# Performance work log

Measured on AMD Instinct MI355X. Metric: run time of the kernel, lower is better.

Reference implementation:

```python
import jax, jax.numpy as jnp
import numpy as np

N_JOINTS = 21
EDGES = np.array([[0,13],[0,1],[0,4],[0,10],[0,7],[13,14],[14,15],[15,16],[1,2],[2,3],[3,17],[4,5],[5,6],[6,18],[10,11],[11,12],[12,19],[7,8],[8,9],[9,20]], dtype=np.int32)


def _build_adj():
    # SemGCN-style adj_mx_from_edges: symmetric adjacency + self loops, row-normalized
    A = np.zeros((N_JOINTS, N_JOINTS), np.float32)
    A[EDGES[:, 0], EDGES[:, 1]] = 1.0
    A = np.maximum(A, A.T)
    A = A + np.eye(N_JOINTS, dtype=np.float32)
    A = A / A.sum(axis=1, keepdims=True)
    return A


def setup_inputs() -> dict:
    key = jax.random.key(0)
    ks = jax.random.split(key, 8)
    B, C, Hm, Wm = 128, 235, 64, 64
    heads, fo = 4, 32
    feature_s = jax.random.normal(ks[0], (B, C, Hm, Wm), jnp.float32)
    target_s = jax.random.uniform(ks[1], (B, N_JOINTS, Hm, Wm), jnp.float32)
    bn_gamma = jnp.ones((N_JOINTS,), jnp.float32)
    bn_beta = jnp.zeros((N_JOINTS,), jnp.float32)
    gat_w = jax.random.normal(ks[2], (C, heads * fo), jnp.float32) * 0.05
    gat_att_src = jax.random.normal(ks[3], (heads, fo), jnp.float32) * 0.1
    gat_att_dst = jax.random.normal(ks[4], (heads, fo), jnp.float32) * 0.1
    gat_bias = jnp.zeros((heads * fo,), jnp.float32)
    cheb_w = jax.random.normal(ks[5], (2, heads * fo, 3), jnp.float32) * 0.05
    cheb_bias = jnp.zeros((3,), jnp.float32)
    # PyG GATConv adds self loops: 20 skeleton edges + 21 self edges = 41
    src = np.concatenate([EDGES[:, 0], np.arange(N_JOINTS, dtype=np.int32)])
    dst = np.concatenate([EDGES[:, 1], np.arange(N_JOINTS, dtype=np.int32)])
    return {
        'feature_s': feature_s, 'target_s': target_s,
        'bn_gamma': bn_gamma, 'bn_beta': bn_beta,
        'gat_w': gat_w, 'gat_att_src': gat_att_src, 'gat_att_dst': gat_att_dst,
        'gat_bias': gat_bias, 'cheb_w': cheb_w, 'cheb_bias': cheb_bias,
        'adj': jnp.asarray(_build_adj()),
        'edge_src': jnp.asarray(src), 'edge_dst': jnp.asarray(dst),
    }


def reference(feature_s, target_s, bn_gamma, bn_beta, gat_w, gat_att_src, gat_att_dst, gat_bias, cheb_w, cheb_bias, adj, edge_src, edge_dst):
    B, C = feature_s.shape[0], feature_s.shape[1]
    N = target_s.shape[1]
    # per-sample query embedding: [B, 21, HW] @ [B, HW, C] -> [B, 21, C]
    f = feature_s.reshape(B, C, -1)
    t = target_s.reshape(B, N, -1)
    q = jnp.einsum('bnp,bcp->bnc', t, f)
    # BatchNorm1d(21), training mode: normalize per joint-channel over (B, C)
    mean = q.mean(axis=(0, 2), keepdims=True)
    var = q.var(axis=(0, 2), keepdims=True)
    q = (q - mean) * jax.lax.rsqrt(var + 1e-5) * bn_gamma[None, :, None] + bn_beta[None, :, None]
    q = jnp.where(q >= 0, q, 0.1 * q)  # LeakyReLU(0.1)
    # GATConv (4 heads, 32 dims, concat) vmapped over batch of identical graphs
    heads, fo = gat_att_src.shape
    h = (q @ gat_w).reshape(B, N, heads, fo)
    a_src = jnp.einsum('bnhf,hf->bnh', h, gat_att_src)
    a_dst = jnp.einsum('bnhf,hf->bnh', h, gat_att_dst)
    e = a_src[:, edge_src] + a_dst[:, edge_dst]           # [B, E, H]
    e = jnp.where(e >= 0, e, 0.2 * e)                     # GAT default negative_slope=0.2
    seg_max = jax.vmap(lambda v: jax.ops.segment_max(v, edge_dst, num_segments=N))
    seg_sum = jax.vmap(lambda v: jax.ops.segment_sum(v, edge_dst, num_segments=N))
    m = seg_max(e)                                        # [B, N, H]
    ex = jnp.exp(e - m[:, edge_dst])
    den = seg_sum(ex)
    alpha = ex / den[:, edge_dst]                         # per-dst softmax
    msg = alpha[..., None] * h[:, edge_src]               # [B, E, H, Fo]
    out = seg_sum(msg.reshape(B, -1, heads * fo))         # [B, N, H*Fo]
    x = out + gat_bias
    # ChebConv K=2 (GraFormer-style): T0 = I, T1 = L = I - D^{-1/2} A D^{-1/2}
    d = jnp.sum(adj, axis=-1) ** -0.5
    L = jnp.eye(N, dtype=adj.dtype) - d[:, None] * adj * d[None, :]
    y = jnp.einsum('bnc,co->bno', x, cheb_w[0]) + jnp.einsum('mn,bnc,co->bmo', L, x, cheb_w[1])
    return y + cheb_bias
```

## Files before the change

kernel.cpp:

```cpp
#include <hip/hip_runtime.h>
#include <hip/hip_bf16.h>

constexpr int B  = 128;
constexpr int C  = 235;
constexpr int N  = 21;
constexpr int HW = 4096;
constexpr int HO = 128;
constexpr int E  = 41;

typedef __attribute__((ext_vector_type(8)))  short  short8;
typedef __attribute__((ext_vector_type(16))) float  f32x16;

__device__ inline unsigned short bf16r(float x) {
    return __bfloat16_as_ushort(__float2bfloat16(x));
}

constexpr int KSPLIT = 8;
constexpr int KRANGE = HW / KSPLIT;

__global__ __launch_bounds__(256) void k1_qgemm(
    const float* __restrict__ f,
    const float* __restrict__ t,
    float* __restrict__ qp)
{
    const int b    = blockIdx.y;
    const int ks   = blockIdx.x;
    const int tid  = threadIdx.x;
    const int wave = tid >> 6;
    const int lane = tid & 63;
    const int l31  = lane & 31;
    const int kh   = lane >> 5;

    const float* fb = f + (size_t)b * C * HW;
    const float* tb = t + (size_t)b * N * HW;

    const int arow = (l31 < N) ? l31 : (N - 1);
    const int c1   = wave * 64 + l31;
    const int c2   = wave * 64 + 32 + l31;
    const int c1c  = (c1 < C) ? c1 : (C - 1);
    const int c2c  = (c2 < C) ? c2 : (C - 1);

    const float* pa = tb + (size_t)arow * HW + kh * 8;
    const float* p1 = fb + (size_t)c1c  * HW + kh * 8;
    const float* p2 = fb + (size_t)c2c  * HW + kh * 8;

    f32x16 acc0 = {};
    f32x16 acc1 = {};

    const int kend = ks * KRANGE + KRANGE;
    #pragma unroll 2
    for (int k = ks * KRANGE; k < kend; k += 16) {
        const float4 alo = *reinterpret_cast<const float4*>(pa + k);
        const float4 ahi = *reinterpret_cast<const float4*>(pa + k + 4);
        const float4 b1l = *reinterpret_cast<const float4*>(p1 + k);
        const float4 b1h = *reinterpret_cast<const float4*>(p1 + k + 4);
        const float4 b2l = *reinterpret_cast<const float4*>(p2 + k);
        const float4 b2h = *reinterpret_cast<const float4*>(p2 + k + 4);

        union { short8 v; unsigned short u[8]; } av, bv1, bv2;
        av.u[0]  = bf16r(alo.x); av.u[1]  = bf16r(alo.y);
        av.u[2]  = bf16r(alo.z); av.u[3]  = bf16r(alo.w);
        av.u[4]  = bf16r(ahi.x); av.u[5]  = bf16r(ahi.y);
        av.u[6]  = bf16r(ahi.z); av.u[7]  = bf16r(ahi.w);
        bv1.u[0] = bf16r(b1l.x); bv1.u[1] = bf16r(b1l.y);
        bv1.u[2] = bf16r(b1l.z); bv1.u[3] = bf16r(b1l.w);
        bv1.u[4] = bf16r(b1h.x); bv1.u[5] = bf16r(b1h.y);
        bv1.u[6] = bf16r(b1h.z); bv1.u[7] = bf16r(b1h.w);
        bv2.u[0] = bf16r(b2l.x); bv2.u[1] = bf16r(b2l.y);
        bv2.u[2] = bf16r(b2l.z); bv2.u[3] = bf16r(b2l.w);
        bv2.u[4] = bf16r(b2h.x); bv2.u[5] = bf16r(b2h.y);
        bv2.u[6] = bf16r(b2h.z); bv2.u[7] = bf16r(b2h.w);

        acc0 = __builtin_amdgcn_mfma_f32_32x32x16_bf16(av.v, bv1.v, acc0, 0, 0, 0);
        acc1 = __builtin_amdgcn_mfma_f32_32x32x16_bf16(av.v, bv2.v, acc1, 0, 0, 0);
    }

    float* qpk = qp + ((size_t)ks * B + b) * N * C;
    #pragma unroll
    for (int reg = 0; reg < 16; reg++) {
        const int row = (reg & 3) + 8 * (reg >> 2) + 4 * kh;
        if (row < N) {
            if (c1 < C) qpk[row * C + c1] = acc0[reg];
            if (c2 < C) qpk[row * C + c2] = acc1[reg];
        }
    }
}

__global__ __launch_bounds__(256) void k1b_reduce(
    const float* __restrict__ qp, float* __restrict__ q)
{
    const int i = blockIdx.x * 256 + threadIdx.x;
    constexpr int S = B * N * C;
    if (i < S) {
        float s = 0.f;
        #pragma unroll
        for (int p = 0; p < KSPLIT; p++) s += qp[(size_t)p * S + i];
        q[i] = s;
    }
}

__global__ __launch_bounds__(256) void k2_bnstats(
    const float* __restrict__ q,
    const float* __restrict__ gamma,
    const float* __restrict__ beta,
    float* __restrict__ stats)
{
    const int n = blockIdx.x;
    const int tid = threadIdx.x;
    float s = 0.f, s2 = 0.f;
    if (tid < C) {
        for (int b = 0; b < B; b++) {
            const float v = q[((size_t)b * N + n) * C + tid];
            s += v; s2 += v * v;
        }
    }
    for (int off = 32; off; off >>= 1) {
        s  += __shfl_down(s,  off);
        s2 += __shfl_down(s2, off);
    }
    __shared__ float rs[4], rs2[4];
    const int wave = tid >> 6, lane = tid & 63;
    if (lane == 0) { rs[wave] = s; rs2[wave] = s2; }
    __syncthreads();
    if (tid == 0) {
        const float S  = rs[0] + rs[1] + rs[2] + rs[3];
        const float S2 = rs2[0] + rs2[1] + rs2[2] + rs2[3];
        const float cnt = (float)(B * C);
        const float mean = S / cnt;
        const float var  = S2 / cnt - mean * mean;
        const float scale = gamma[n] * rsqrtf(var + 1e-5f);
        stats[2 * n]     = scale;
        stats[2 * n + 1] = beta[n] - mean * scale;
    }
}

__global__ __launch_bounds__(256) void k3_tail(
    const float* __restrict__ q,
    const float* __restrict__ stats,
    const float* __restrict__ gatw,
    const float* __restrict__ attsrc,
    const float* __restrict__ attdst,
    const float* __restrict__ gatbias,
    const float* __restrict__ chebw,
    const float* __restrict__ chebbias,
    const float* __restrict__ adj,
    const int* __restrict__ esrc,
    const int* __restrict__ edst,
    float* __restrict__ out)
{
    __shared__ float ql[N][C + 1];
    __shared__ float Wl[48][HO];
    __shared__ float hl[N][HO];
    __shared__ float xl[N][HO];
    __shared__ float asrcl[N][4], adstl[N][4];
    __shared__ float el[E][4], alphal[E][4];
    __shared__ float mx[N][4], den[N][4];
    __shared__ float zl[N][3], t0l[N][3], dsl[N];
    __shared__ int esl[E], edl[E];

    const int b = blockIdx.x;
    const int tid = threadIdx.x;

    for (int v = tid; v < N * C; v += 256) {
        const int n = v / C, c = v % C;
        float x = q[((size_t)b * N + n) * C + c];
        x = x * stats[2 * n] + stats[2 * n + 1];
        ql[n][c] = (x >= 0.f) ? x : 0.1f * x;
    }
    if (tid < E) { esl[tid] = esrc[tid]; edl[tid] = edst[tid]; }
    for (int v = tid; v < N * HO; v += 256) hl[v >> 7][v & 127] = 0.f;
    __syncthreads();

    for (int k0 = 0; k0 < C; k0 += 48) {
        const int kc = (C - k0) < 48 ? (C - k0) : 48;
        for (int v = tid; v < kc * HO; v += 256) {
            const int kk = v >> 7, o = v & 127;
            Wl[kk][o] = gatw[(size_t)(k0 + kk) * HO + o];
        }
        __syncthreads();
        for (int idx = tid; idx < N * HO; idx += 256) {
            const int n = idx >> 7, o = idx & 127;
            float s = hl[n][o];
            for (int kk = 0; kk < kc; kk++)
                s += ql[n][k0 + kk] * Wl[kk][o];
            hl[n][o] = s;
        }
        __syncthreads();
    }

    if (tid < N * 4) {
        const int n = tid >> 2, h = tid & 3;
        float ss = 0.f, sd = 0.f;
        for (int fo = 0; fo < 32; fo++) {
            const float hv = hl[n][h * 32 + fo];
            ss += hv * attsrc[h * 32 + fo];
            sd += hv * attdst[h * 32 + fo];
        }
        asrcl[n][h] = ss; adstl[n][h] = sd;
    }
    __syncthreads();
    if (tid < E * 4) {
        const int e = tid >> 2, h = tid & 3;
        const float v = asrcl[esl[e]][h] + adstl[edl[e]][h];
        el[e][h] = (v >= 0.f) ? v : 0.2f * v;
    }
    __syncthreads();
    if (tid < N * 4) {
        const int n = tid >> 2, h = tid & 3;
        float m = -1e30f;
        for (int e = 0; e < E; e++)
            if (edl[e] == n) m = fmaxf(m, el[e][h]);
        mx[n][h] = m;
    }
    __syncthreads();
    if (tid < E * 4) {
        const int e = tid >> 2, h = tid & 3;
        el[e][h] = __expf(el[e][h] - mx[edl[e]][h]);
    }
    __syncthreads();
    if (tid < N * 4) {
        const int n = tid >> 2, h = tid & 3;
        float s = 0.f;
        for (int e = 0; e < E; e++)
            if (edl[e] == n) s += el[e][h];
        den[n][h] = s;
    }
    __syncthreads();
    if (tid < E * 4) {
        const int e = tid >> 2, h = tid & 3;
        alphal[e][h] = el[e][h] / den[edl[e]][h];
    }
    __syncthreads();

    for (int idx = tid; idx < N * HO; idx += 256) {
        const int n = idx >> 7, o = idx & 127, h = o >> 5;
        float s = 0.f;
        for (int e = 0; e < E; e++)
            if (edl[e] == n) s += alphal[e][h] * hl[esl[e]][o];
        xl[n][o] = s + gatbias[o];
    }
    if (tid < N) {
        float s = 0.f;
        for (int j = 0; j < N; j++) s += adj[tid * N + j];
        dsl[tid] = rsqrtf(s);
    }
    __syncthreads();

    if (tid < N * 3) {
        const int n = tid / 3, o = tid % 3;
        float s0 = 0.f, sz = 0.f;
        for (int c2 = 0; c2 < HO; c2++) {
            const float xv = xl[n][c2];
            s0 += xv * chebw[(size_t)c2 * 3 + o];
            sz += xv * chebw[(size_t)(HO + c2) * 3 + o];
        }
        t0l[n][o] = s0; zl[n][o] = sz;
    }
    __syncthreads();
    if (tid < N * 3) {
        const int m = tid / 3, o = tid % 3;
        float s = t0l[m][o] + zl[m][o];
        for (int n2 = 0; n2 < N; n2++)
            s -= dsl[m] * adj[m * N + n2] * dsl[n2] * zl[n2][o];
        out[(size_t)b * N * 3 + tid] = s + chebbias[o];
    }
}

extern "C" void kernel_launch(void* const* d_in, const int* in_sizes, int n_in,
                              void* d_out, int out_size, void* d_ws, size_t ws_size,
                              hipStream_t stream) {
    const float* feature  = (const float*)d_in[0];
    const float* target   = (const float*)d_in[1];
    const float* gamma    = (const float*)d_in[2];
    const float* beta     = (const float*)d_in[3];
    const float* gatw     = (const float*)d_in[4];
    const float* attsrc   = (const float*)d_in[5];
    const float* attdst   = (const float*)d_in[6];
    const float* gatbias  = (const float*)d_in[7];
    const float* chebw    = (const float*)d_in[8];
    const float* chebbias = (const float*)d_in[9];
    const float* adj      = (const float*)d_in[10];
    const int*   esrc     = (const int*)d_in[11];
    const int*   edst     = (const int*)d_in[12];

    constexpr int QS = B * N * C;
    float* qp    = (float*)d_ws;
    float* q     = qp + (size_t)KSPLIT * QS;
    float* stats = q + QS;
    float* out   = (float*)d_out;

    hipLaunchKernelGGL(k1_qgemm, dim3(KSPLIT, B), dim3(256), 0, stream,
                       feature, target, qp);
    hipLaunchKernelGGL(k1b_reduce, dim3((QS + 255) / 256), dim3(256), 0, stream, qp, q);
    hipLaunchKernelGGL(k2_bnstats, dim3(N), dim3(256), 0, stream, q, gamma, beta, stats);
    hipLaunchKernelGGL(k3_tail, dim3(B), dim3(256), 0, stream,
                       q, stats, gatw, attsrc, attdst, gatbias, chebw, chebbias,
                       adj, esrc, edst, out);
}
```

Measured before the change: 191.0 us.

## Stage bf16 tiles in LDS with swizzle and split channel blocks across workgroups

The batched GEMM kernel now loads 256-wide K stages of feature and target rows cooperatively, converts them to bf16 and stores them in XOR-swizzled shared memory. Each wave then reads its MFMA operands from LDS. The channel dimension is split into four 64-wide blocks across workgroups, with a remapped block index so neighbouring blocks fall on different batches. The K split drops to 2, and the two wave-level K halves write separate partial slots, giving four partial buffers to reduce. The aim is coalesced global loads and less redundant per-lane conversion, at the cost of extra barriers and no overlap between loading and compute.

```diff
diff --git a/kernel.cpp b/kernel.cpp
--- a/kernel.cpp
+++ b/kernel.cpp
@@ -15,74 +15,97 @@
     return __bfloat16_as_ushort(__float2bfloat16(x));
 }
 
-constexpr int KSPLIT = 8;
+constexpr int KSPLIT = 2;
 constexpr int KRANGE = HW / KSPLIT;
+constexpr int KSTAGE = 256;
+constexpr int NSLOT  = KSPLIT * 2;
 
 __global__ __launch_bounds__(256) void k1_qgemm(
     const float* __restrict__ f,
     const float* __restrict__ t,
     float* __restrict__ qp)
 {
-    const int b    = blockIdx.y;
-    const int ks   = blockIdx.x;
+    __shared__ short8 fls[64 * 32];
+    __shared__ short8 tls[21 * 32];
+
+    const int j = blockIdx.x;
+    const int logical = (j & 7) * 128 + (j >> 3);
+    const int cblk = logical & 3;
+    const int ks   = (logical >> 2) & 1;
+    const int b    = logical >> 3;
+
     const int tid  = threadIdx.x;
     const int wave = tid >> 6;
     const int lane = tid & 63;
     const int l31  = lane & 31;
     const int kh   = lane >> 5;
-
+    const int tc   = wave & 1;
+    const int kw   = wave >> 1;
+
+    const int c0 = cblk * 64;
     const float* fb = f + (size_t)b * C * HW;
     const float* tb = t + (size_t)b * N * HW;
 
+    f32x16 acc = {};
+
     const int arow = (l31 < N) ? l31 : (N - 1);
-    const int c1   = wave * 64 + l31;
-    const int c2   = wave * 64 + 32 + l31;
-    const int c1c  = (c1 < C) ? c1 : (C - 1);
-    const int c2c  = (c2 < C) ? c2 : (C - 1);
-
-    const float* pa = tb + (size_t)arow * HW + kh * 8;
-    const float* p1 = fb + (size_t)c1c  * HW + kh * 8;
-    const float* p2 = fb + (size_t)c2c  * HW + kh * 8;
-
-    f32x16 acc0 = {};
-    f32x16 acc1 = {};
-
-    const int kend = ks * KRANGE + KRANGE;
-    #pragma unroll 2
-    for (int k = ks * KRANGE; k < kend; k += 16) {
-        const float4 alo = *reinterpret_cast<const float4*>(pa + k);
-        const float4 ahi = *reinterpret_cast<const float4*>(pa + k + 4);
-        const float4 b1l = *reinterpret_cast<const float4*>(p1 + k);
-        const float4 b1h = *reinterpret_cast<const float4*>(p1 + k + 4);
-        const float4 b2l = *reinterpret_cast<const float4*>(p2 + k);
-        const float4 b2h = *reinterpret_cast<const float4*>(p2 + k + 4);
-
-        union { short8 v; unsigned short u[8]; } av, bv1, bv2;
-        av.u[0]  = bf16r(alo.x); av.u[1]  = bf16r(alo.y);
-        av.u[2]  = bf16r(alo.z); av.u[3]  = bf16r(alo.w);
-        av.u[4]  = bf16r(ahi.x); av.u[5]  = bf16r(ahi.y);
-        av.u[6]  = bf16r(ahi.z); av.u[7]  = bf16r(ahi.w);
-        bv1.u[0] = bf16r(b1l.x); bv1.u[1] = bf16r(b1l.y);
-        bv1.u[2] = bf16r(b1l.z); bv1.u[3] = bf16r(b1l.w);
-        bv1.u[4] = bf16r(b1h.x); bv1.u[5] = bf16r(b1h.y);
-        bv1.u[6] = bf16r(b1h.z); bv1.u[7] = bf16r(b1h.w);
-        bv2.u[0] = bf16r(b2l.x); bv2.u[1] = bf16r(b2l.y);
-        bv2.u[2] = bf16r(b2l.z); bv2.u[3] = bf16r(b2l.w);
-        bv2.u[4] = bf16r(b2h.x); bv2.u[5] = bf16r(b2h.y);
-        bv2.u[6] = bf16r(b2h.z); bv2.u[7] = bf16r(b2h.w);
-
-        acc0 = __builtin_amdgcn_mfma_f32_32x32x16_bf16(av.v, bv1.v, acc0, 0, 0, 0);
-        acc1 = __builtin_amdgcn_mfma_f32_32x32x16_bf16(av.v, bv2.v, acc1, 0, 0, 0);
-    }
-
-    float* qpk = qp + ((size_t)ks * B + b) * N * C;
+    const int frow = tc * 32 + l31;
+
+    for (int st = 0; st < KRANGE / KSTAGE; ++st) {
+        const int kst = ks * KRANGE + st * KSTAGE;
+        __syncthreads();
+        #pragma unroll
+        for (int i = 0; i < 8; i++) {
+            const int v = tid + i * 256;
+            const int r = v >> 5;
+            const int s = v & 31;
+            const int c = c0 + r;
+            float4 x0 = make_float4(0.f, 0.f, 0.f, 0.f);
+            float4 x1 = make_float4(0.f, 0.f, 0.f, 0.f);
+            if (c < C) {
+                const float* src = fb + (size_t)c * HW + kst + s * 8;
+                x0 = *reinterpret_cast<const float4*>(src);
+                x1 = *reinterpret_cast<const float4*>(src + 4);
+            }
+            union { short8 v8; unsigned short u[8]; } pk;
+            pk.u[0] = bf16r(x0.x); pk.u[1] = bf16r(x0.y);
+            pk.u[2] = bf16r(x0.z); pk.u[3] = bf16r(x0.w);
+            pk.u[4] = bf16r(x1.x); pk.u[5] = bf16r(x1.y);
+            pk.u[6] = bf16r(x1.z); pk.u[7] = bf16r(x1.w);
+            fls[r * 32 + (s ^ (r & 15))] = pk.v8;
+        }
+        for (int v = tid; v < N * 32; v += 256) {
+            const int r = v >> 5;
+            const int s = v & 31;
+            const float* src = tb + (size_t)r * HW + kst + s * 8;
+            const float4 x0 = *reinterpret_cast<const float4*>(src);
+            const float4 x1 = *reinterpret_cast<const float4*>(src + 4);
+            union { short8 v8; unsigned short u[8]; } pk;
+            pk.u[0] = bf16r(x0.x); pk.u[1] = bf16r(x0.y);
+            pk.u[2] = bf16r(x0.z); pk.u[3] = bf16r(x0.w);
+            pk.u[4] = bf16r(x1.x); pk.u[5] = bf16r(x1.y);
+            pk.u[6] = bf16r(x1.z); pk.u[7] = bf16r(x1.w);
+            tls[r * 32 + (s ^ (r & 15))] = pk.v8;
+        }
+        __syncthreads();
+
+        #pragma unroll
+        for (int it = 0; it < 8; it++) {
+            const int kslot = kw * 16 + it * 2 + kh;
+            const short8 av = tls[arow * 32 + (kslot ^ (arow & 15))];
+            const short8 bv = fls[frow * 32 + (kslot ^ (frow & 15))];
+            acc = __builtin_amdgcn_mfma_f32_32x32x16_bf16(av, bv, acc, 0, 0, 0);
+        }
+    }
+
+    const int slot = ks * 2 + kw;
+    float* qpk = qp + ((size_t)slot * B + b) * N * C;
+    const int col = c0 + tc * 32 + l31;
     #pragma unroll
     for (int reg = 0; reg < 16; reg++) {
         const int row = (reg & 3) + 8 * (reg >> 2) + 4 * kh;
-        if (row < N) {
-            if (c1 < C) qpk[row * C + c1] = acc0[reg];
-            if (c2 < C) qpk[row * C + c2] = acc1[reg];
-        }
+        if (row < N && col < C)
+            qpk[row * C + col] = acc[reg];
     }
 }
 
@@ -94,7 +117,7 @@
     if (i < S) {
         float s = 0.f;
         #pragma unroll
-        for (int p = 0; p < KSPLIT; p++) s += qp[(size_t)p * S + i];
+        for (int p = 0; p < NSLOT; p++) s += qp[(size_t)p * S + i];
         q[i] = s;
     }
 }
@@ -241,7 +264,7 @@
     }
     if (tid < N) {
         float s = 0.f;
-        for (int j = 0; j < N; j++) s += adj[tid * N + j];
+        for (int j2 = 0; j2 < N; j2++) s += adj[tid * N + j2];
         dsl[tid] = rsqrtf(s);
     }
     __syncthreads();
@@ -285,11 +308,11 @@
 
     constexpr int QS = B * N * C;
     float* qp    = (float*)d_ws;
-    float* q     = qp + (size_t)KSPLIT * QS;
+    float* q     = qp + (size_t)NSLOT * QS;
     float* stats = q + QS;
     float* out   = (float*)d_out;
 
-    hipLaunchKernelGGL(k1_qgemm, dim3(KSPLIT, B), dim3(256), 0, stream,
+    hipLaunchKernelGGL(k1_qgemm, dim3(4 * KSPLIT * B), dim3(256), 0, stream,
                        feature, target, qp);
     hipLaunchKernelGGL(k1b_reduce, dim3((QS + 255) / 256), dim3(256), 0, stream, qp, q);
     hipLaunchKernelGGL(k2_bnstats, dim3(N), dim3(256), 0, stream, q, gamma, beta, stats);
```

Measured after the change: 193.5 us. No clear change (+1.4%).

## Split GEMM columns across blocks with XCD swizzle and fuse split-K reduce with BN stats

Applied to the files above, without the earlier changes.

The q GEMM now launches twice as many blocks. Each wave handles one 32-column tile instead of two, and the 1D grid index is remapped so that consecutive logical blocks land on the same XCD. The main loop adds register double-buffering of the next loads. The split-K reduction and per-batch BatchNorm partial sums are fused into one per-batch kernel. The final cross-batch stats reduction is folded into the tail kernel, which removes a separate launch and a second pass over q. The cost is that each tail block redundantly reduces the 128 partial stats, and the A-matrix loads are now duplicated across column groups.

```diff
diff --git a/kernel.cpp b/kernel.cpp
--- a/kernel.cpp
+++ b/kernel.cpp
@@ -17,14 +17,19 @@
 
 constexpr int KSPLIT = 8;
 constexpr int KRANGE = HW / KSPLIT;
+constexpr int NSLOT  = KSPLIT;
 
 __global__ __launch_bounds__(256) void k1_qgemm(
     const float* __restrict__ f,
     const float* __restrict__ t,
     float* __restrict__ qp)
 {
-    const int b    = blockIdx.y;
-    const int ks   = blockIdx.x;
+    const int j = blockIdx.x;
+    const int logical = (j & 7) * 256 + (j >> 3);
+    const int cg = logical & 1;
+    const int ks = (logical >> 1) & 7;
+    const int b  = logical >> 4;
+
     const int tid  = threadIdx.x;
     const int wave = tid >> 6;
     const int lane = tid & 63;
@@ -35,108 +40,92 @@
     const float* tb = t + (size_t)b * N * HW;
 
     const int arow = (l31 < N) ? l31 : (N - 1);
-    const int c1   = wave * 64 + l31;
-    const int c2   = wave * 64 + 32 + l31;
-    const int c1c  = (c1 < C) ? c1 : (C - 1);
-    const int c2c  = (c2 < C) ? c2 : (C - 1);
+    const int col  = cg * 128 + wave * 32 + l31;
+    const int colc = (col < C) ? col : (C - 1);
 
     const float* pa = tb + (size_t)arow * HW + kh * 8;
-    const float* p1 = fb + (size_t)c1c  * HW + kh * 8;
-    const float* p2 = fb + (size_t)c2c  * HW + kh * 8;
-
-    f32x16 acc0 = {};
-    f32x16 acc1 = {};
-
-    const int kend = ks * KRANGE + KRANGE;
-    #pragma unroll 2
-    for (int k = ks * KRANGE; k < kend; k += 16) {
-        const float4 alo = *reinterpret_cast<const float4*>(pa + k);
-        const float4 ahi = *reinterpret_cast<const float4*>(pa + k + 4);
-        const float4 b1l = *reinterpret_cast<const float4*>(p1 + k);
-        const float4 b1h = *reinterpret_cast<const float4*>(p1 + k + 4);
-        const float4 b2l = *reinterpret_cast<const float4*>(p2 + k);
-        const float4 b2h = *reinterpret_cast<const float4*>(p2 + k + 4);
-
-        union { short8 v; unsigned short u[8]; } av, bv1, bv2;
-        av.u[0]  = bf16r(alo.x); av.u[1]  = bf16r(alo.y);
-        av.u[2]  = bf16r(alo.z); av.u[3]  = bf16r(alo.w);
-        av.u[4]  = bf16r(ahi.x); av.u[5]  = bf16r(ahi.y);
-        av.u[6]  = bf16r(ahi.z); av.u[7]  = bf16r(ahi.w);
-        bv1.u[0] = bf16r(b1l.x); bv1.u[1] = bf16r(b1l.y);
-        bv1.u[2] = bf16r(b1l.z); bv1.u[3] = bf16r(b1l.w);
-        bv1.u[4] = bf16r(b1h.x); bv1.u[5] = bf16r(b1h.y);
-        bv1.u[6] = bf16r(b1h.z); bv1.u[7] = bf16r(b1h.w);
-        bv2.u[0] = bf16r(b2l.x); bv2.u[1] = bf16r(b2l.y);
-        bv2.u[2] = bf16r(b2l.z); bv2.u[3] = bf16r(b2l.w);
-        bv2.u[4] = bf16r(b2h.x); bv2.u[5] = bf16r(b2h.y);
-        bv2.u[6] = bf16r(b2h.z); bv2.u[7] = bf16r(b2h.w);
-
-        acc0 = __builtin_amdgcn_mfma_f32_32x32x16_bf16(av.v, bv1.v, acc0, 0, 0, 0);
-        acc1 = __builtin_amdgcn_mfma_f32_32x32x16_bf16(av.v, bv2.v, acc1, 0, 0, 0);
+    const float* pb = fb + (size_t)colc * HW + kh * 8;
+
+    f32x16 acc = {};
+    const int kbase = ks * KRANGE;
+    const int kend  = kbase + KRANGE;
+
+    float4 A0 = *reinterpret_cast<const float4*>(pa + kbase);
+    float4 A1 = *reinterpret_cast<const float4*>(pa + kbase + 4);
+    float4 B0 = *reinterpret_cast<const float4*>(pb + kbase);
+    float4 B1 = *reinterpret_cast<const float4*>(pb + kbase + 4);
+
+    #pragma unroll 4
+    for (int k = kbase; k < kend; k += 16) {
+        const float4 a0 = A0, a1 = A1, b0 = B0, b1 = B1;
+        if (k + 16 < kend) {
+            A0 = *reinterpret_cast<const float4*>(pa + k + 16);
+            A1 = *reinterpret_cast<const float4*>(pa + k + 20);
+            B0 = *reinterpret_cast<const float4*>(pb + k + 16);
+            B1 = *reinterpret_cast<const float4*>(pb + k + 20);
+        }
+        union { short8 v; unsigned short u[8]; } av, bv;
+        av.u[0] = bf16r(a0.x); av.u[1] = bf16r(a0.y);
+        av.u[2] = bf16r(a0.z); av.u[3] = bf16r(a0.w);
+        av.u[4] = bf16r(a1.x); av.u[5] = bf16r(a1.y);
+        av.u[6] = bf16r(a1.z); av.u[7] = bf16r(a1.w);
+        bv.u[0] = bf16r(b0.x); bv.u[1] = bf16r(b0.y);
+        bv.u[2] = bf16r(b0.z); bv.u[3] = bf16r(b0.w);
+        bv.u[4] = bf16r(b1.x); bv.u[5] = bf16r(b1.y);
+        bv.u[6] = bf16r(b1.z); bv.u[7] = bf16r(b1.w);
+        acc = __builtin_amdgcn_mfma_f32_32x32x16_bf16(av.v, bv.v, acc, 0, 0, 0);
     }
 
     float* qpk = qp + ((size_t)ks * B + b) * N * C;
     #pragma unroll
     for (int reg = 0; reg < 16; reg++) {
         const int row = (reg & 3) + 8 * (reg >> 2) + 4 * kh;
-        if (row < N) {
-            if (c1 < C) qpk[row * C + c1] = acc0[reg];
-            if (c2 < C) qpk[row * C + c2] = acc1[reg];
-        }
-    }
-}
-
-__global__ __launch_bounds__(256) void k1b_reduce(
-    const float* __restrict__ qp, float* __restrict__ q)
+        if (row < N && col < C)
+            qpk[row * C + col] = acc[reg];
+    }
+}
+
+__global__ __launch_bounds__(256) void k1b_bn(
+    const float* __restrict__ qp,
+    float* __restrict__ q,
+    float* __restrict__ bnp)
 {
-    const int i = blockIdx.x * 256 + threadIdx.x;
+    const int b    = blockIdx.x;
+    const int tid  = threadIdx.x;
+    const int wave = tid >> 6;
+    const int lane = tid & 63;
+    __shared__ float rs[N][4], rs2[N][4];
     constexpr int S = B * N * C;
-    if (i < S) {
-        float s = 0.f;
-        #pragma unroll
-        for (int p = 0; p < KSPLIT; p++) s += qp[(size_t)p * S + i];
-        q[i] = s;
-    }
-}
-
-__global__ __launch_bounds__(256) void k2_bnstats(
+
+    for (int n = 0; n < N; ++n) {
+        float v = 0.f;
+        const int idx = (b * N + n) * C + tid;
+        if (tid < C) {
+            #pragma unroll
+            for (int p = 0; p < NSLOT; p++) v += qp[(size_t)p * S + idx];
+            q[idx] = v;
+        }
+        float s = v, s2 = v * v;
+        for (int off = 32; off; off >>= 1) {
+            s  += __shfl_down(s,  off);
+            s2 += __shfl_down(s2, off);
+        }
+        if (lane == 0) { rs[n][wave] = s; rs2[n][wave] = s2; }
+    }
+    __syncthreads();
+    if (tid < N) {
+        const float S1 = rs[tid][0] + rs[tid][1] + rs[tid][2] + rs[tid][3];
+        const float S2 = rs2[tid][0] + rs2[tid][1] + rs2[tid][2] + rs2[tid][3];
+        bnp[(b * N + tid) * 2]     = S1;
+        bnp[(b * N + tid) * 2 + 1] = S2;
+    }
+}
+
+__global__ __launch_bounds__(256) void k3_tail(
     const float* __restrict__ q,
+    const float* __restrict__ bnp,
     const float* __restrict__ gamma,
     const float* __restrict__ beta,
-    float* __restrict__ stats)
-{
-    const int n = blockIdx.x;
-    const int tid = threadIdx.x;
-    float s = 0.f, s2 = 0.f;
-    if (tid < C) {
-        for (int b = 0; b < B; b++) {
-            const float v = q[((size_t)b * N + n) * C + tid];
-            s += v; s2 += v * v;
-        }
-    }
-    for (int off = 32; off; off >>= 1) {
-        s  += __shfl_down(s,  off);
-        s2 += __shfl_down(s2, off);
-    }
-    __shared__ float rs[4], rs2[4];
-    const int wave = tid >> 6, lane = tid & 63;
-    if (lane == 0) { rs[wave] = s; rs2[wave] = s2; }
-    __syncthreads();
-    if (tid == 0) {
-        const float S  = rs[0] + rs[1] + rs[2] + rs[3];
-        const float S2 = rs2[0] + rs2[1] + rs2[2] + rs2[3];
-        const float cnt = (float)(B * C);
-        const float mean = S / cnt;
-        const float var  = S2 / cnt - mean * mean;
-        const float scale = gamma[n] * rsqrtf(var + 1e-5f);
-        stats[2 * n]     = scale;
-        stats[2 * n + 1] = beta[n] - mean * scale;
-    }
-}
-
-__global__ __launch_bounds__(256) void k3_tail(
-    const float* __restrict__ q,
-    const float* __restrict__ stats,
     const float* __restrict__ gatw,
     const float* __restrict__ attsrc,
     const float* __restrict__ attdst,
@@ -152,6 +141,7 @@
     __shared__ float Wl[48][HO];
     __shared__ float hl[N][HO];
     __shared__ float xl[N][HO];
+    __shared__ float stl[N][2];
     __shared__ float asrcl[N][4], adstl[N][4];
     __shared__ float el[E][4], alphal[E][4];
     __shared__ float mx[N][4], den[N][4];
@@ -161,13 +151,28 @@
     const int b = blockIdx.x;
     const int tid = threadIdx.x;
 
+    if (tid < N) {
+        float S1 = 0.f, S2 = 0.f;
+        for (int bb = 0; bb < B; bb++) {
+            S1 += bnp[(bb * N + tid) * 2];
+            S2 += bnp[(bb * N + tid) * 2 + 1];
+        }
+        const float cnt  = (float)(B * C);
+        const float mean = S1 / cnt;
+        const float var  = S2 / cnt - mean * mean;
+        const float sc   = gamma[tid] * rsqrtf(var + 1e-5f);
+        stl[tid][0] = sc;
+        stl[tid][1] = beta[tid] - mean * sc;
+    }
+    if (tid < E) { esl[tid] = esrc[tid]; edl[tid] = edst[tid]; }
+    __syncthreads();
+
     for (int v = tid; v < N * C; v += 256) {
         const int n = v / C, c = v % C;
         float x = q[((size_t)b * N + n) * C + c];
-        x = x * stats[2 * n] + stats[2 * n + 1];
+        x = x * stl[n][0] + stl[n][1];
         ql[n][c] = (x >= 0.f) ? x : 0.1f * x;
     }
-    if (tid < E) { esl[tid] = esrc[tid]; edl[tid] = edst[tid]; }
     for (int v = tid; v < N * HO; v += 256) hl[v >> 7][v & 127] = 0.f;
     __syncthreads();
 
@@ -241,7 +246,7 @@
     }
     if (tid < N) {
         float s = 0.f;
-        for (int j = 0; j < N; j++) s += adj[tid * N + j];
+        for (int j2 = 0; j2 < N; j2++) s += adj[tid * N + j2];
         dsl[tid] = rsqrtf(s);
     }
     __syncthreads();
@@ -284,16 +289,15 @@
     const int*   edst     = (const int*)d_in[12];
 
     constexpr int QS = B * N * C;
-    float* qp    = (float*)d_ws;
-    float* q     = qp + (size_t)KSPLIT * QS;
-    float* stats = q + QS;
-    float* out   = (float*)d_out;
-
-    hipLaunchKernelGGL(k1_qgemm, dim3(KSPLIT, B), dim3(256), 0, stream,
+    float* qp  = (float*)d_ws;
+    float* q   = qp + (size_t)NSLOT * QS;
+    float* bnp = q + QS;
+    float* out = (float*)d_out;
+
+    hipLaunchKernelGGL(k1_qgemm, dim3(2 * KSPLIT * B), dim3(256), 0, stream,
                        feature, target, qp);
-    hipLaunchKernelGGL(k1b_reduce, dim3((QS + 255) / 256), dim3(256), 0, stream, qp, q);
-    hipLaunchKernelGGL(k2_bnstats, dim3(N), dim3(256), 0, stream, q, gamma, beta, stats);
+    hipLaunchKernelGGL(k1b_bn, dim3(B), dim3(256), 0, stream, qp, q, bnp);
     hipLaunchKernelGGL(k3_tail, dim3(B), dim3(256), 0, stream,
-                       q, stats, gatw, attsrc, attdst, gatbias, chebw, chebbias,
-                       adj, esrc, edst, out);
-}
+                       q, bnp, gamma, beta, gatw, attsrc, attdst, gatbias,
+                       chebw, chebbias, adj, esrc, edst, out);
+}
```

Measured after the change: 224.2 us. 17.4% more time.
